# Kernel tuning notes

Hardware: AMD Instinct MI355X
Metric: run time of the kernel (lower is better)

The kernel has to match this reference:

```python
import jax, jax.numpy as jnp
import numpy as np

N_QUERY = 1024
N_REF = 100000
D_LATENT = 128
K = 8


def setup_inputs() -> dict:
    key = jax.random.key(0)
    k1, k2 = jax.random.split(key)
    x = jax.random.normal(k1, (N_QUERY, D_LATENT), dtype=jnp.float32)
    base_data = jax.random.normal(k2, (N_REF, D_LATENT), dtype=jnp.float32)
    return {"x": x, "base_data": base_data, "k": K}


def reference(x, base_data, k):
    base_norm = jnp.sum(base_data * base_data, axis=1)        # [N_ref]
    x_norm = jnp.sum(x * x, axis=1)                           # [N_q]
    # [N_q, N_ref] distance matrix
    diffs = base_norm[None, :] + x_norm[:, None] - 2.0 * jnp.einsum(
        "qd,rd->qr", x, base_data
    )
    diffs = jnp.sqrt(diffs)
    # top-k SMALLEST distances, sorted ascending (torch.topk largest=False)
    neg_top, _ = jax.lax.top_k(-diffs, k)
    return (-neg_top).astype(jnp.float32)
```

## Files before the change

### kernel.cpp

```cpp
#include <hip/hip_runtime.h>
#include <math.h>

#define NQ 1024
#define NR 100000
#define D  128
#define K  8
#define NCH   64
#define CHUNK 1563
#define TR    32
#define NT    49
#define QPW   32

typedef __attribute__((ext_vector_type(8))) short short8;
typedef __attribute__((ext_vector_type(4))) float f32x4;

static __device__ __forceinline__ unsigned short f2bf(float f) {
    unsigned int u = __float_as_uint(f);
    return (unsigned short)((u + 0x7FFFu + ((u >> 16) & 1u)) >> 16);
}
static __device__ __forceinline__ float bf2f(unsigned short h) {
    return __uint_as_float(((unsigned int)h) << 16);
}

__device__ __forceinline__ void topk_insert(float (&t)[K], float d) {
    if (d < t[K - 1]) {
#pragma unroll
        for (int j = K - 1; j > 0; --j)
            t[j] = (d >= t[j]) ? t[j] : ((d < t[j - 1]) ? t[j - 1] : d);
        t[0] = (d < t[0]) ? d : t[0];
    }
}

__global__ __launch_bounds__(512, 2) void knn_mfma(const float* __restrict__ x,
                                                   const float* __restrict__ base,
                                                   float* __restrict__ cand) {
    __shared__ unsigned short lhs[2][TR * 128];
    __shared__ unsigned short lls[2][TR * 128];
    __shared__ float lbn[2][TR];

    const int tid  = threadIdx.x;
    const int lane = tid & 63;
    const int w    = tid >> 6;
    const int lm   = lane & 15;
    const int kg   = lane >> 4;
    const int qb   = blockIdx.x & 3;
    const int rc   = blockIdx.x >> 2;
    const int r0   = rc * CHUNK;
    const int rend = (r0 + CHUNK < NR) ? (r0 + CHUNK) : NR;

    short8 Bh[2][4], Bl[2][4];
    float  xn[2];
#pragma unroll
    for (int qt = 0; qt < 2; ++qt) {
        const int q = qb * 256 + w * QPW + qt * 16 + lm;
        float s2 = 0.f;
#pragma unroll
        for (int s = 0; s < 4; ++s) {
            const float4 a = *(const float4*)(x + (size_t)q * D + s * 32 + kg * 8);
            const float4 b = *(const float4*)(x + (size_t)q * D + s * 32 + kg * 8 + 4);
            float v[8] = {a.x, a.y, a.z, a.w, b.x, b.y, b.z, b.w};
            short8 hh, ll;
#pragma unroll
            for (int j = 0; j < 8; ++j) {
                s2 = fmaf(v[j], v[j], s2);
                const float m2 = -2.f * v[j];
                const unsigned short h = f2bf(m2);
                const float r = m2 - bf2f(h);
                hh[j] = (short)h;
                ll[j] = (short)f2bf(r);
            }
            Bh[qt][s] = hh; Bl[qt][s] = ll;
        }
        s2 += __shfl_xor(s2, 16, 64);
        s2 += __shfl_xor(s2, 32, 64);
        xn[qt] = s2;
    }

    const int srow = tid >> 4;
    const int scol = tid & 15;

    auto convert_store = [&](const float (&v)[8], int gr, int buf) {
        float s2 = 0.f;
        short8 hh, ll;
#pragma unroll
        for (int j = 0; j < 8; ++j) {
            s2 = fmaf(v[j], v[j], s2);
            const unsigned short h = f2bf(v[j]);
            const float r = v[j] - bf2f(h);
            hh[j] = (short)h;
            ll[j] = (short)f2bf(r);
        }
        s2 += __shfl_xor(s2, 1, 64);
        s2 += __shfl_xor(s2, 2, 64);
        s2 += __shfl_xor(s2, 4, 64);
        s2 += __shfl_xor(s2, 8, 64);
        const int idx = srow * 128 + 8 * (scol ^ (srow & 15));
        *(short8*)&lhs[buf][idx] = hh;
        *(short8*)&lls[buf][idx] = ll;
        if (scol == 0) lbn[buf][srow] = (gr < rend) ? s2 : INFINITY;
    };

    {
        const int gr = r0 + srow;
        float v[8] = {0, 0, 0, 0, 0, 0, 0, 0};
        if (gr < NR) {
            const float4 a = *(const float4*)(base + (size_t)gr * D + scol * 8);
            const float4 b = *(const float4*)(base + (size_t)gr * D + scol * 8 + 4);
            v[0] = a.x; v[1] = a.y; v[2] = a.z; v[3] = a.w;
            v[4] = b.x; v[5] = b.y; v[6] = b.z; v[7] = b.w;
        }
        convert_store(v, gr, 0);
    }
    __syncthreads();

    float t0[K], t1[K];
#pragma unroll
    for (int j = 0; j < K; ++j) { t0[j] = INFINITY; t1[j] = INFINITY; }

    int cur = 0;
    for (int ti = 0; ti < NT; ++ti) {
        float pv[8] = {0, 0, 0, 0, 0, 0, 0, 0};
        int pgr = NR;
        if (ti + 1 < NT) {
            pgr = r0 + (ti + 1) * TR + srow;
            if (pgr < NR) {
                const float4 a = *(const float4*)(base + (size_t)pgr * D + scol * 8);
                const float4 b = *(const float4*)(base + (size_t)pgr * D + scol * 8 + 4);
                pv[0] = a.x; pv[1] = a.y; pv[2] = a.z; pv[3] = a.w;
                pv[4] = b.x; pv[5] = b.y; pv[6] = b.z; pv[7] = b.w;
            }
        }

#pragma unroll
        for (int rt = 0; rt < 2; ++rt) {
            const f32x4 bn4 = *(const f32x4*)&lbn[cur][rt * 16 + kg * 4];
            f32x4 acc0 = {0.f, 0.f, 0.f, 0.f};
            f32x4 acc1 = {0.f, 0.f, 0.f, 0.f};
#pragma unroll
            for (int s = 0; s < 4; ++s) {
                const int idx = (rt * 16 + lm) * 128 + 8 * ((s * 4 + kg) ^ lm);
                const short8 Ah = *(const short8*)&lhs[cur][idx];
                const short8 Al = *(const short8*)&lls[cur][idx];
                acc0 = __builtin_amdgcn_mfma_f32_16x16x32_bf16(Ah, Bh[0][s], acc0, 0, 0, 0);
                acc1 = __builtin_amdgcn_mfma_f32_16x16x32_bf16(Ah, Bh[1][s], acc1, 0, 0, 0);
                acc0 = __builtin_amdgcn_mfma_f32_16x16x32_bf16(Ah, Bl[0][s], acc0, 0, 0, 0);
                acc1 = __builtin_amdgcn_mfma_f32_16x16x32_bf16(Ah, Bl[1][s], acc1, 0, 0, 0);
                acc0 = __builtin_amdgcn_mfma_f32_16x16x32_bf16(Al, Bh[0][s], acc0, 0, 0, 0);
                acc1 = __builtin_amdgcn_mfma_f32_16x16x32_bf16(Al, Bh[1][s], acc1, 0, 0, 0);
            }
#pragma unroll
            for (int j = 0; j < 4; ++j) {
                topk_insert(t0, acc0[j] + bn4[j]);
                topk_insert(t1, acc1[j] + bn4[j]);
            }
        }

        if (ti + 1 < NT) convert_store(pv, pgr, cur ^ 1);
        __syncthreads();
        cur ^= 1;
    }

#pragma unroll
    for (int st = 16; st <= 32; st <<= 1) {
        float o0[K], o1[K];
#pragma unroll
        for (int j = 0; j < K; ++j) {
            o0[j] = __shfl_xor(t0[j], st, 64);
            o1[j] = __shfl_xor(t1[j], st, 64);
        }
#pragma unroll
        for (int j = 0; j < K; ++j) { topk_insert(t0, o0[j]); topk_insert(t1, o1[j]); }
    }

    if (kg == 0) {
#pragma unroll
        for (int qt = 0; qt < 2; ++qt) {
            const int q = qb * 256 + w * QPW + qt * 16 + lm;
            float* cp = cand + ((size_t)q * NCH + rc) * K;
#pragma unroll
            for (int j = 0; j < K; ++j) {
                const float d2 = (qt ? t1[j] : t0[j]) + xn[qt];
                cp[j] = sqrtf(fmaxf(d2, 0.f));
            }
        }
    }
}

__global__ __launch_bounds__(256, 4) void knn_merge(const float* __restrict__ cand,
                                                    float* __restrict__ out) {
    const int q = blockIdx.x * blockDim.x + threadIdx.x;
    if (q >= NQ) return;
    const float* cp = cand + (size_t)q * (NCH * K);
    float t[K];
#pragma unroll
    for (int j = 0; j < K; ++j) t[j] = INFINITY;
    for (int i = 0; i < NCH * K; i += 4) {
        const float4 v = *(const float4*)(cp + i);
        topk_insert(t, v.x); topk_insert(t, v.y);
        topk_insert(t, v.z); topk_insert(t, v.w);
    }
#pragma unroll
    for (int j = 0; j < K; ++j) out[(size_t)q * K + j] = t[j];
}

extern "C" void kernel_launch(void* const* d_in, const int* in_sizes, int n_in,
                              void* d_out, int out_size, void* d_ws, size_t ws_size,
                              hipStream_t stream) {
    const float* x    = (const float*)d_in[0];
    const float* base = (const float*)d_in[1];
    float* out  = (float*)d_out;
    float* cand = (float*)d_ws;

    knn_mfma<<<4 * NCH, 512, 0, stream>>>(x, base, cand);
    knn_merge<<<(NQ + 255) / 256, 256, 0, stream>>>(cand, out);
}
```

Baseline: 288.1 us.

## Pre-split base into bf16 hi/lo tiles and stream via global_load_lds

Adds a prep kernel that converts the base matrix once into swizzled bf16 hi/lo tiles plus row norms in workspace. The main kernel then copies the pre-converted tiles straight into LDS with global_load_lds, so it no longer does per-block conversion or the register staging round trip. Each block now handles 64 queries per wave (4 query tiles) across 125 reference chunks, which raises reuse of each loaded base tile. It adds an extra kernel pass plus about 51MB of workspace traffic, and falls back to the old path when the workspace is too small.

```diff
diff --git a/kernel.cpp b/kernel.cpp
--- a/kernel.cpp
+++ b/kernel.cpp
@@ -5,14 +5,17 @@
 #define NR 100000
 #define D  128
 #define K  8
-#define NCH   64
-#define CHUNK 1563
-#define TR    32
-#define NT    49
-#define QPW   32
+#define TR 32
+#define NTILES 3125
+#define NCH 125
+#define TPC 25
+#define NQG 2
 
 typedef __attribute__((ext_vector_type(8))) short short8;
 typedef __attribute__((ext_vector_type(4))) float f32x4;
+typedef unsigned int u32;
+typedef __attribute__((address_space(1))) const u32 gu32;
+typedef __attribute__((address_space(3))) u32 lu32;
 
 static __device__ __forceinline__ unsigned short f2bf(float f) {
     unsigned int u = __float_as_uint(f);
@@ -31,9 +34,185 @@
     }
 }
 
-__global__ __launch_bounds__(512, 2) void knn_mfma(const float* __restrict__ x,
-                                                   const float* __restrict__ base,
-                                                   float* __restrict__ cand) {
+
+__global__ __launch_bounds__(512, 4) void knn_prep(const float* __restrict__ base,
+                                                   unsigned short* __restrict__ bhi,
+                                                   unsigned short* __restrict__ blo,
+                                                   float* __restrict__ bn) {
+    const int t   = blockIdx.x;
+    const int tid = threadIdx.x;
+    const int r   = tid >> 4;
+    const int c   = tid & 15;
+    const int row = t * TR + r;
+
+    const float4 a = *(const float4*)(base + (size_t)row * D + c * 8);
+    const float4 b = *(const float4*)(base + (size_t)row * D + c * 8 + 4);
+    float v[8] = {a.x, a.y, a.z, a.w, b.x, b.y, b.z, b.w};
+    float s2 = 0.f;
+    short8 hh, ll;
+#pragma unroll
+    for (int j = 0; j < 8; ++j) {
+        s2 = fmaf(v[j], v[j], s2);
+        const unsigned short h = f2bf(v[j]);
+        const float res = v[j] - bf2f(h);
+        hh[j] = (short)h;
+        ll[j] = (short)f2bf(res);
+    }
+    s2 += __shfl_xor(s2, 1, 64);
+    s2 += __shfl_xor(s2, 2, 64);
+    s2 += __shfl_xor(s2, 4, 64);
+    s2 += __shfl_xor(s2, 8, 64);
+
+    const size_t o = (size_t)t * (TR * 128) + r * 128 + 8 * (c ^ (r & 15));
+    *(short8*)(bhi + o) = hh;
+    *(short8*)(blo + o) = ll;
+    if (c == 0) bn[row] = s2;
+}
+
+__global__ __launch_bounds__(512, 2) void knn_mfma2(const float* __restrict__ x,
+                                                    const unsigned short* __restrict__ bhi,
+                                                    const unsigned short* __restrict__ blo,
+                                                    const float* __restrict__ bn,
+                                                    float* __restrict__ cand) {
+    __shared__ unsigned short lhs[2][TR * 128];
+    __shared__ unsigned short lls[2][TR * 128];
+
+    const int tid  = threadIdx.x;
+    const int lane = tid & 63;
+    const int w    = tid >> 6;
+    const int lm   = lane & 15;
+    const int kg   = lane >> 4;
+    const int qb   = blockIdx.x & 1;
+    const int rc   = blockIdx.x >> 1;
+    const int t0   = rc * TPC;
+
+    short8 Bh[4][4], Bl[4][4];
+    float  xn[4];
+#pragma unroll
+    for (int qt = 0; qt < 4; ++qt) {
+        const int q = qb * 512 + w * 64 + qt * 16 + lm;
+        float s2 = 0.f;
+#pragma unroll
+        for (int s = 0; s < 4; ++s) {
+            const float4 a = *(const float4*)(x + (size_t)q * D + s * 32 + kg * 8);
+            const float4 b = *(const float4*)(x + (size_t)q * D + s * 32 + kg * 8 + 4);
+            float v[8] = {a.x, a.y, a.z, a.w, b.x, b.y, b.z, b.w};
+            short8 hh, ll;
+#pragma unroll
+            for (int j = 0; j < 8; ++j) {
+                s2 = fmaf(v[j], v[j], s2);
+                const float m2 = -2.f * v[j];
+                const unsigned short h = f2bf(m2);
+                const float res = m2 - bf2f(h);
+                hh[j] = (short)h;
+                ll[j] = (short)f2bf(res);
+            }
+            Bh[qt][s] = hh; Bl[qt][s] = ll;
+        }
+        s2 += __shfl_xor(s2, 16, 64);
+        s2 += __shfl_xor(s2, 32, 64);
+        xn[qt] = s2;
+    }
+
+    auto stage = [&](int ti, int buf) {
+        const size_t gb = (size_t)(t0 + ti) * (TR * 128);
+        unsigned short* lh = &lhs[buf][w * 512];
+        unsigned short* ll = &lls[buf][w * 512];
+        const unsigned short* gh = bhi + gb + w * 512 + lane * 8;
+        const unsigned short* gl = blo + gb + w * 512 + lane * 8;
+        __builtin_amdgcn_global_load_lds((gu32*)gh, (lu32*)lh, 16, 0, 0);
+        __builtin_amdgcn_global_load_lds((gu32*)gl, (lu32*)ll, 16, 0, 0);
+    };
+
+    float tk[4][K];
+#pragma unroll
+    for (int qt = 0; qt < 4; ++qt)
+#pragma unroll
+        for (int j = 0; j < K; ++j) tk[qt][j] = INFINITY;
+
+    stage(0, 0);
+    __syncthreads();
+
+    int cur = 0;
+    for (int ti = 0; ti < TPC; ++ti) {
+        if (ti + 1 < TPC) stage(ti + 1, cur ^ 1);
+
+#pragma unroll
+        for (int rt = 0; rt < 2; ++rt) {
+            const f32x4 bn4 = *(const f32x4*)(bn + (size_t)(t0 + ti) * TR + rt * 16 + kg * 4);
+            f32x4 acc[4];
+#pragma unroll
+            for (int qt = 0; qt < 4; ++qt) acc[qt] = (f32x4){0.f, 0.f, 0.f, 0.f};
+#pragma unroll
+            for (int s = 0; s < 4; ++s) {
+                const int idx = (rt * 16 + lm) * 128 + 8 * ((s * 4 + kg) ^ lm);
+                const short8 Ah = *(const short8*)&lhs[cur][idx];
+                const short8 Al = *(const short8*)&lls[cur][idx];
+#pragma unroll
+                for (int qt = 0; qt < 4; ++qt) {
+                    acc[qt] = __builtin_amdgcn_mfma_f32_16x16x32_bf16(Ah, Bh[qt][s], acc[qt], 0, 0, 0);
+                    acc[qt] = __builtin_amdgcn_mfma_f32_16x16x32_bf16(Ah, Bl[qt][s], acc[qt], 0, 0, 0);
+                    acc[qt] = __builtin_amdgcn_mfma_f32_16x16x32_bf16(Al, Bh[qt][s], acc[qt], 0, 0, 0);
+                }
+            }
+#pragma unroll
+            for (int qt = 0; qt < 4; ++qt)
+#pragma unroll
+                for (int j = 0; j < 4; ++j) topk_insert(tk[qt], acc[qt][j] + bn4[j]);
+        }
+
+        __syncthreads();
+        cur ^= 1;
+    }
+
+#pragma unroll
+    for (int st = 16; st <= 32; st <<= 1) {
+#pragma unroll
+        for (int qt = 0; qt < 4; ++qt) {
+            float o[K];
+#pragma unroll
+            for (int j = 0; j < K; ++j) o[j] = __shfl_xor(tk[qt][j], st, 64);
+#pragma unroll
+            for (int j = 0; j < K; ++j) topk_insert(tk[qt], o[j]);
+        }
+    }
+
+    if (kg == 0) {
+#pragma unroll
+        for (int qt = 0; qt < 4; ++qt) {
+            const int q = qb * 512 + w * 64 + qt * 16 + lm;
+            float* cp = cand + ((size_t)q * NCH + rc) * K;
+#pragma unroll
+            for (int j = 0; j < K; ++j)
+                cp[j] = sqrtf(fmaxf(tk[qt][j] + xn[qt], 0.f));
+        }
+    }
+}
+
+__global__ __launch_bounds__(256, 4) void knn_merge2(const float* __restrict__ cand,
+                                                     float* __restrict__ out) {
+    const int q = blockIdx.x * blockDim.x + threadIdx.x;
+    if (q >= NQ) return;
+    const float* cp = cand + (size_t)q * (NCH * K);
+    float t[K];
+#pragma unroll
+    for (int j = 0; j < K; ++j) t[j] = INFINITY;
+    for (int i = 0; i < NCH * K; i += 4) {
+        const float4 v = *(const float4*)(cp + i);
+        topk_insert(t, v.x); topk_insert(t, v.y);
+        topk_insert(t, v.z); topk_insert(t, v.w);
+    }
+#pragma unroll
+    for (int j = 0; j < K; ++j) out[(size_t)q * K + j] = t[j];
+}
+
+#define FB_NCH   64
+#define FB_CHUNK 1563
+#define FB_NT    49
+
+__global__ __launch_bounds__(512, 2) void knn_mfma_fb(const float* __restrict__ x,
+                                                      const float* __restrict__ base,
+                                                      float* __restrict__ cand) {
     __shared__ unsigned short lhs[2][TR * 128];
     __shared__ unsigned short lls[2][TR * 128];
     __shared__ float lbn[2][TR];
@@ -45,14 +224,14 @@
     const int kg   = lane >> 4;
     const int qb   = blockIdx.x & 3;
     const int rc   = blockIdx.x >> 2;
-    const int r0   = rc * CHUNK;
-    const int rend = (r0 + CHUNK < NR) ? (r0 + CHUNK) : NR;
+    const int r0   = rc * FB_CHUNK;
+    const int rend = (r0 + FB_CHUNK < NR) ? (r0 + FB_CHUNK) : NR;
 
     short8 Bh[2][4], Bl[2][4];
     float  xn[2];
 #pragma unroll
     for (int qt = 0; qt < 2; ++qt) {
-        const int q = qb * 256 + w * QPW + qt * 16 + lm;
+        const int q = qb * 256 + w * 32 + qt * 16 + lm;
         float s2 = 0.f;
 #pragma unroll
         for (int s = 0; s < 4; ++s) {
@@ -65,9 +244,9 @@
                 s2 = fmaf(v[j], v[j], s2);
                 const float m2 = -2.f * v[j];
                 const unsigned short h = f2bf(m2);
-                const float r = m2 - bf2f(h);
+                const float res = m2 - bf2f(h);
                 hh[j] = (short)h;
-                ll[j] = (short)f2bf(r);
+                ll[j] = (short)f2bf(res);
             }
             Bh[qt][s] = hh; Bl[qt][s] = ll;
         }
@@ -86,9 +265,9 @@
         for (int j = 0; j < 8; ++j) {
             s2 = fmaf(v[j], v[j], s2);
             const unsigned short h = f2bf(v[j]);
-            const float r = v[j] - bf2f(h);
+            const float res = v[j] - bf2f(h);
             hh[j] = (short)h;
-            ll[j] = (short)f2bf(r);
+            ll[j] = (short)f2bf(res);
         }
         s2 += __shfl_xor(s2, 1, 64);
         s2 += __shfl_xor(s2, 2, 64);
@@ -113,15 +292,15 @@
     }
     __syncthreads();
 
-    float t0[K], t1[K];
-#pragma unroll
-    for (int j = 0; j < K; ++j) { t0[j] = INFINITY; t1[j] = INFINITY; }
+    float t0a[K], t1a[K];
+#pragma unroll
+    for (int j = 0; j < K; ++j) { t0a[j] = INFINITY; t1a[j] = INFINITY; }
 
     int cur = 0;
-    for (int ti = 0; ti < NT; ++ti) {
+    for (int ti = 0; ti < FB_NT; ++ti) {
         float pv[8] = {0, 0, 0, 0, 0, 0, 0, 0};
         int pgr = NR;
-        if (ti + 1 < NT) {
+        if (ti + 1 < FB_NT) {
             pgr = r0 + (ti + 1) * TR + srow;
             if (pgr < NR) {
                 const float4 a = *(const float4*)(base + (size_t)pgr * D + scol * 8);
@@ -150,12 +329,12 @@
             }
 #pragma unroll
             for (int j = 0; j < 4; ++j) {
-                topk_insert(t0, acc0[j] + bn4[j]);
-                topk_insert(t1, acc1[j] + bn4[j]);
-            }
-        }
-
-        if (ti + 1 < NT) convert_store(pv, pgr, cur ^ 1);
+                topk_insert(t0a, acc0[j] + bn4[j]);
+                topk_insert(t1a, acc1[j] + bn4[j]);
+            }
+        }
+
+        if (ti + 1 < FB_NT) convert_store(pv, pgr, cur ^ 1);
         __syncthreads();
         cur ^= 1;
     }
@@ -165,36 +344,36 @@
         float o0[K], o1[K];
 #pragma unroll
         for (int j = 0; j < K; ++j) {
-            o0[j] = __shfl_xor(t0[j], st, 64);
-            o1[j] = __shfl_xor(t1[j], st, 64);
-        }
-#pragma unroll
-        for (int j = 0; j < K; ++j) { topk_insert(t0, o0[j]); topk_insert(t1, o1[j]); }
+            o0[j] = __shfl_xor(t0a[j], st, 64);
+            o1[j] = __shfl_xor(t1a[j], st, 64);
+        }
+#pragma unroll
+        for (int j = 0; j < K; ++j) { topk_insert(t0a, o0[j]); topk_insert(t1a, o1[j]); }
     }
 
     if (kg == 0) {
 #pragma unroll
         for (int qt = 0; qt < 2; ++qt) {
-            const int q = qb * 256 + w * QPW + qt * 16 + lm;
-            float* cp = cand + ((size_t)q * NCH + rc) * K;
+            const int q = qb * 256 + w * 32 + qt * 16 + lm;
+            float* cp = cand + ((size_t)q * FB_NCH + rc) * K;
 #pragma unroll
             for (int j = 0; j < K; ++j) {
-                const float d2 = (qt ? t1[j] : t0[j]) + xn[qt];
+                const float d2 = (qt ? t1a[j] : t0a[j]) + xn[qt];
                 cp[j] = sqrtf(fmaxf(d2, 0.f));
             }
         }
     }
 }
 
-__global__ __launch_bounds__(256, 4) void knn_merge(const float* __restrict__ cand,
-                                                    float* __restrict__ out) {
+__global__ __launch_bounds__(256, 4) void knn_merge_fb(const float* __restrict__ cand,
+                                                       float* __restrict__ out) {
     const int q = blockIdx.x * blockDim.x + threadIdx.x;
     if (q >= NQ) return;
-    const float* cp = cand + (size_t)q * (NCH * K);
+    const float* cp = cand + (size_t)q * (FB_NCH * K);
     float t[K];
 #pragma unroll
     for (int j = 0; j < K; ++j) t[j] = INFINITY;
-    for (int i = 0; i < NCH * K; i += 4) {
+    for (int i = 0; i < FB_NCH * K; i += 4) {
         const float4 v = *(const float4*)(cp + i);
         topk_insert(t, v.x); topk_insert(t, v.y);
         topk_insert(t, v.z); topk_insert(t, v.w);
@@ -208,9 +387,25 @@
                               hipStream_t stream) {
     const float* x    = (const float*)d_in[0];
     const float* base = (const float*)d_in[1];
-    float* out  = (float*)d_out;
-    float* cand = (float*)d_ws;
-
-    knn_mfma<<<4 * NCH, 512, 0, stream>>>(x, base, cand);
-    knn_merge<<<(NQ + 255) / 256, 256, 0, stream>>>(cand, out);
-}
+    float* out = (float*)d_out;
+
+    const size_t OFF_BLO  = 25600000;
+    const size_t OFF_BN   = 51200000;
+    const size_t OFF_CAND = 51600384;
+    const size_t NEED     = OFF_CAND + (size_t)NQ * NCH * K * 4;
+
+    if (ws_size >= NEED) {
+        unsigned short* bhi = (unsigned short*)d_ws;
+        unsigned short* blo = (unsigned short*)((char*)d_ws + OFF_BLO);
+        float* bn   = (float*)((char*)d_ws + OFF_BN);
+        float* cand = (float*)((char*)d_ws + OFF_CAND);
+
+        knn_prep<<<NTILES, 512, 0, stream>>>(base, bhi, blo, bn);
+        knn_mfma2<<<NQG * NCH, 512, 0, stream>>>(x, bhi, blo, bn, cand);
+        knn_merge2<<<(NQ + 255) / 256, 256, 0, stream>>>(cand, out);
+    } else {
+        float* cand = (float*)d_ws;
+        knn_mfma_fb<<<4 * FB_NCH, 512, 0, stream>>>(x, base, cand);
+        knn_merge_fb<<<(NQ + 255) / 256, 256, 0, stream>>>(cand, out);
+    }
+}
```

After: 370.6 us. 1.29x slower.

## Widen per-wave query tile to 64 and split reference rows into 125 even chunks

Applied to the files above, without the earlier changes.

Each wave now holds 4 query tiles (64 queries) in registers instead of 2, so every reference tile loaded into LDS is reused across twice as many queries and base data is streamed only twice instead of four times. Reference rows are split into 125 chunks of exactly 800 rows, which removes the bounds checks and infinity padding. The grid is now 250 blocks with occupancy 1 instead of 256 blocks with occupancy 2. Register pressure roughly doubles (B fragments, accumulators, top-k lists), which risks spills and leaves fewer waves to hide latency, and the merge kernel now scans 1000 candidates per query instead of 512.

```diff
diff --git a/kernel.cpp b/kernel.cpp
--- a/kernel.cpp
+++ b/kernel.cpp
@@ -5,11 +5,11 @@
 #define NR 100000
 #define D  128
 #define K  8
-#define NCH   64
-#define CHUNK 1563
-#define TR    32
-#define NT    49
-#define QPW   32
+#define TR 32
+#define NCH   125
+#define CHUNK 800
+#define TPC   25
+#define NQG   2
 
 typedef __attribute__((ext_vector_type(8))) short short8;
 typedef __attribute__((ext_vector_type(4))) float f32x4;
@@ -31,9 +31,9 @@
     }
 }
 
-__global__ __launch_bounds__(512, 2) void knn_mfma(const float* __restrict__ x,
-                                                   const float* __restrict__ base,
-                                                   float* __restrict__ cand) {
+__global__ __launch_bounds__(512, 1) void knn_mfma3(const float* __restrict__ x,
+                                                    const float* __restrict__ base,
+                                                    float* __restrict__ cand) {
     __shared__ unsigned short lhs[2][TR * 128];
     __shared__ unsigned short lls[2][TR * 128];
     __shared__ float lbn[2][TR];
@@ -43,16 +43,15 @@
     const int w    = tid >> 6;
     const int lm   = lane & 15;
     const int kg   = lane >> 4;
-    const int qb   = blockIdx.x & 3;
-    const int rc   = blockIdx.x >> 2;
+    const int qb   = blockIdx.x & 1;
+    const int rc   = blockIdx.x >> 1;
     const int r0   = rc * CHUNK;
-    const int rend = (r0 + CHUNK < NR) ? (r0 + CHUNK) : NR;
-
-    short8 Bh[2][4], Bl[2][4];
-    float  xn[2];
-#pragma unroll
-    for (int qt = 0; qt < 2; ++qt) {
-        const int q = qb * 256 + w * QPW + qt * 16 + lm;
+
+    short8 Bh[4][4], Bl[4][4];
+    float  xn[4];
+#pragma unroll
+    for (int qt = 0; qt < 4; ++qt) {
+        const int q = qb * 512 + w * 64 + qt * 16 + lm;
         float s2 = 0.f;
 #pragma unroll
         for (int s = 0; s < 4; ++s) {
@@ -65,9 +64,9 @@
                 s2 = fmaf(v[j], v[j], s2);
                 const float m2 = -2.f * v[j];
                 const unsigned short h = f2bf(m2);
-                const float r = m2 - bf2f(h);
+                const float res = m2 - bf2f(h);
                 hh[j] = (short)h;
-                ll[j] = (short)f2bf(r);
+                ll[j] = (short)f2bf(res);
             }
             Bh[qt][s] = hh; Bl[qt][s] = ll;
         }
@@ -79,16 +78,16 @@
     const int srow = tid >> 4;
     const int scol = tid & 15;
 
-    auto convert_store = [&](const float (&v)[8], int gr, int buf) {
+    auto convert_store = [&](const float (&v)[8], int buf) {
         float s2 = 0.f;
         short8 hh, ll;
 #pragma unroll
         for (int j = 0; j < 8; ++j) {
             s2 = fmaf(v[j], v[j], s2);
             const unsigned short h = f2bf(v[j]);
-            const float r = v[j] - bf2f(h);
+            const float res = v[j] - bf2f(h);
             hh[j] = (short)h;
-            ll[j] = (short)f2bf(r);
+            ll[j] = (short)f2bf(res);
         }
         s2 += __shfl_xor(s2, 1, 64);
         s2 += __shfl_xor(s2, 2, 64);
@@ -97,97 +96,90 @@
         const int idx = srow * 128 + 8 * (scol ^ (srow & 15));
         *(short8*)&lhs[buf][idx] = hh;
         *(short8*)&lls[buf][idx] = ll;
-        if (scol == 0) lbn[buf][srow] = (gr < rend) ? s2 : INFINITY;
+        if (scol == 0) lbn[buf][srow] = s2;
     };
 
     {
-        const int gr = r0 + srow;
-        float v[8] = {0, 0, 0, 0, 0, 0, 0, 0};
-        if (gr < NR) {
-            const float4 a = *(const float4*)(base + (size_t)gr * D + scol * 8);
-            const float4 b = *(const float4*)(base + (size_t)gr * D + scol * 8 + 4);
-            v[0] = a.x; v[1] = a.y; v[2] = a.z; v[3] = a.w;
-            v[4] = b.x; v[5] = b.y; v[6] = b.z; v[7] = b.w;
-        }
-        convert_store(v, gr, 0);
+        const float* bp = base + (size_t)(r0 + srow) * D + scol * 8;
+        const float4 a = *(const float4*)(bp);
+        const float4 b = *(const float4*)(bp + 4);
+        const float v[8] = {a.x, a.y, a.z, a.w, b.x, b.y, b.z, b.w};
+        convert_store(v, 0);
     }
     __syncthreads();
 
-    float t0[K], t1[K];
-#pragma unroll
-    for (int j = 0; j < K; ++j) { t0[j] = INFINITY; t1[j] = INFINITY; }
+    float tk[4][K];
+#pragma unroll
+    for (int qt = 0; qt < 4; ++qt)
+#pragma unroll
+        for (int j = 0; j < K; ++j) tk[qt][j] = INFINITY;
 
     int cur = 0;
-    for (int ti = 0; ti < NT; ++ti) {
-        float pv[8] = {0, 0, 0, 0, 0, 0, 0, 0};
-        int pgr = NR;
-        if (ti + 1 < NT) {
-            pgr = r0 + (ti + 1) * TR + srow;
-            if (pgr < NR) {
-                const float4 a = *(const float4*)(base + (size_t)pgr * D + scol * 8);
-                const float4 b = *(const float4*)(base + (size_t)pgr * D + scol * 8 + 4);
-                pv[0] = a.x; pv[1] = a.y; pv[2] = a.z; pv[3] = a.w;
-                pv[4] = b.x; pv[5] = b.y; pv[6] = b.z; pv[7] = b.w;
-            }
+    for (int ti = 0; ti < TPC; ++ti) {
+        float pv[8];
+        if (ti + 1 < TPC) {
+            const float* bp = base + (size_t)(r0 + (ti + 1) * TR + srow) * D + scol * 8;
+            const float4 a = *(const float4*)(bp);
+            const float4 b = *(const float4*)(bp + 4);
+            pv[0] = a.x; pv[1] = a.y; pv[2] = a.z; pv[3] = a.w;
+            pv[4] = b.x; pv[5] = b.y; pv[6] = b.z; pv[7] = b.w;
         }
 
 #pragma unroll
         for (int rt = 0; rt < 2; ++rt) {
             const f32x4 bn4 = *(const f32x4*)&lbn[cur][rt * 16 + kg * 4];
-            f32x4 acc0 = {0.f, 0.f, 0.f, 0.f};
-            f32x4 acc1 = {0.f, 0.f, 0.f, 0.f};
+            f32x4 acc[4];
+#pragma unroll
+            for (int qt = 0; qt < 4; ++qt) acc[qt] = (f32x4){0.f, 0.f, 0.f, 0.f};
 #pragma unroll
             for (int s = 0; s < 4; ++s) {
                 const int idx = (rt * 16 + lm) * 128 + 8 * ((s * 4 + kg) ^ lm);
                 const short8 Ah = *(const short8*)&lhs[cur][idx];
                 const short8 Al = *(const short8*)&lls[cur][idx];
-                acc0 = __builtin_amdgcn_mfma_f32_16x16x32_bf16(Ah, Bh[0][s], acc0, 0, 0, 0);
-                acc1 = __builtin_amdgcn_mfma_f32_16x16x32_bf16(Ah, Bh[1][s], acc1, 0, 0, 0);
-                acc0 = __builtin_amdgcn_mfma_f32_16x16x32_bf16(Ah, Bl[0][s], acc0, 0, 0, 0);
-                acc1 = __builtin_amdgcn_mfma_f32_16x16x32_bf16(Ah, Bl[1][s], acc1, 0, 0, 0);
-                acc0 = __builtin_amdgcn_mfma_f32_16x16x32_bf16(Al, Bh[0][s], acc0, 0, 0, 0);
-                acc1 = __builtin_amdgcn_mfma_f32_16x16x32_bf16(Al, Bh[1][s], acc1, 0, 0, 0);
+#pragma unroll
+                for (int qt = 0; qt < 4; ++qt) {
+                    acc[qt] = __builtin_amdgcn_mfma_f32_16x16x32_bf16(Ah, Bh[qt][s], acc[qt], 0, 0, 0);
+                    acc[qt] = __builtin_amdgcn_mfma_f32_16x16x32_bf16(Ah, Bl[qt][s], acc[qt], 0, 0, 0);
+                    acc[qt] = __builtin_amdgcn_mfma_f32_16x16x32_bf16(Al, Bh[qt][s], acc[qt], 0, 0, 0);
+                }
             }
 #pragma unroll
-            for (int j = 0; j < 4; ++j) {
-                topk_insert(t0, acc0[j] + bn4[j]);
-                topk_insert(t1, acc1[j] + bn4[j]);
-            }
-        }
-
-        if (ti + 1 < NT) convert_store(pv, pgr, cur ^ 1);
+            for (int qt = 0; qt < 4; ++qt)
+#pragma unroll
+                for (int j = 0; j < 4; ++j) topk_insert(tk[qt], acc[qt][j] + bn4[j]);
+        }
+
+        if (ti + 1 < TPC) convert_store(pv, cur ^ 1);
         __syncthreads();
         cur ^= 1;
     }
 
 #pragma unroll
     for (int st = 16; st <= 32; st <<= 1) {
-        float o0[K], o1[K];
-#pragma unroll
-        for (int j = 0; j < K; ++j) {
-            o0[j] = __shfl_xor(t0[j], st, 64);
-            o1[j] = __shfl_xor(t1[j], st, 64);
-        }
-#pragma unroll
-        for (int j = 0; j < K; ++j) { topk_insert(t0, o0[j]); topk_insert(t1, o1[j]); }
+#pragma unroll
+        for (int qt = 0; qt < 4; ++qt) {
+            float o[K];
+#pragma unroll
+            for (int j = 0; j < K; ++j) o[j] = __shfl_xor(tk[qt][j], st, 64);
+#pragma unroll
+            for (int j = 0; j < K; ++j) topk_insert(tk[qt], o[j]);
+        }
     }
 
     if (kg == 0) {
 #pragma unroll
-        for (int qt = 0; qt < 2; ++qt) {
-            const int q = qb * 256 + w * QPW + qt * 16 + lm;
+        for (int qt = 0; qt < 4; ++qt) {
+            const int q = qb * 512 + w * 64 + qt * 16 + lm;
             float* cp = cand + ((size_t)q * NCH + rc) * K;
 #pragma unroll
-            for (int j = 0; j < K; ++j) {
-                const float d2 = (qt ? t1[j] : t0[j]) + xn[qt];
-                cp[j] = sqrtf(fmaxf(d2, 0.f));
-            }
-        }
-    }
-}
-
-__global__ __launch_bounds__(256, 4) void knn_merge(const float* __restrict__ cand,
-                                                    float* __restrict__ out) {
+            for (int j = 0; j < K; ++j)
+                cp[j] = sqrtf(fmaxf(tk[qt][j] + xn[qt], 0.f));
+        }
+    }
+}
+
+__global__ __launch_bounds__(256, 4) void knn_merge3(const float* __restrict__ cand,
+                                                     float* __restrict__ out) {
     const int q = blockIdx.x * blockDim.x + threadIdx.x;
     if (q >= NQ) return;
     const float* cp = cand + (size_t)q * (NCH * K);
@@ -211,6 +203,6 @@
     float* out  = (float*)d_out;
     float* cand = (float*)d_ws;
 
-    knn_mfma<<<4 * NCH, 512, 0, stream>>>(x, base, cand);
-    knn_merge<<<(NQ + 255) / 256, 256, 0, stream>>>(cand, out);
-}
+    knn_mfma3<<<NQG * NCH, 512, 0, stream>>>(x, base, cand);
+    knn_merge3<<<(NQ + 255) / 256, 256, 0, stream>>>(cand, out);
+}
```

Result: slower. 348.2 us (+20.9%).
